# Kernel tuning notes

Hardware: AMD Instinct MI355X
Metric: run time of the kernel (lower is better)

## Reference

```python
import jax, jax.numpy as jnp
import numpy as np

B, C_IN, IMG, P, G, E, H = 4, 3, 576, 16, 36, 768, 12
T = G * G  # 1296 tokens
HD = E // H  # 64
LN_EPS = 1e-5


def layer_norm(x, g, b):
    mu = jnp.mean(x, axis=-1, keepdims=True)
    var = jnp.mean((x - mu) ** 2, axis=-1, keepdims=True)
    return (x - mu) * jax.lax.rsqrt(var + LN_EPS) * g + b


def setup_inputs() -> dict:
    key = jax.random.key(0)
    ks = jax.random.split(key, 12)
    s = lambda *sh: 0.02
    return {
        "x": jax.random.normal(ks[0], (B, C_IN, IMG, IMG), jnp.float32),
        "conv_w": jax.random.normal(ks[1], (E, C_IN, P, P), jnp.float32) * 0.02,
        "conv_b": jnp.zeros((E,), jnp.float32),
        "wq": jax.random.normal(ks[2], (E, E), jnp.float32) * 0.02,
        "wk": jax.random.normal(ks[3], (E, E), jnp.float32) * 0.02,
        "wv": jax.random.normal(ks[4], (E, E), jnp.float32) * 0.02,
        "wo": jax.random.normal(ks[5], (E, E), jnp.float32) * 0.02,
        "bo": jnp.zeros((E,), jnp.float32),
        "w1": jax.random.normal(ks[6], (E, 4 * E), jnp.float32) * 0.02,
        "b1": jnp.zeros((4 * E,), jnp.float32),
        "w2": jax.random.normal(ks[7], (4 * E, E), jnp.float32) * 0.02,
        "b2": jnp.zeros((E,), jnp.float32),
        "ln1_g": jnp.ones((E,), jnp.float32),
        "ln1_b": jnp.zeros((E,), jnp.float32),
        "ln2_g": jnp.ones((E,), jnp.float32),
        "ln2_b": jnp.zeros((E,), jnp.float32),
    }


def reference(x, conv_w, conv_b, wq, wk, wv, wo, bo, w1, b1, w2, b2,
              ln1_g, ln1_b, ln2_g, ln2_b):
    # --- patch embed: stride==kernel conv as patch reshape + einsum ---
    xr = x.reshape(B, C_IN, G, P, G, P)  # b c i p j q
    tok = jnp.einsum('bcipjq,ecpq->bije', xr, conv_w) + conv_b
    tok = tok.reshape(B, T, E)  # row-major (i,j) matches flatten(2).transpose

    # --- causal multi-head attention (scale uses n_embd, as in source) ---
    h = layer_norm(tok, ln1_g, ln1_b)
    q = (h @ wq).reshape(B, T, H, HD)
    k = (h @ wk).reshape(B, T, H, HD)
    v = (h @ wv).reshape(B, T, H, HD)
    scores = jnp.einsum('bqhd,bkhd->bhqk', q, k) * (E ** -0.5)
    mask = jnp.tril(jnp.ones((T, T), bool))
    scores = jnp.where(mask, scores, -jnp.inf)
    attn = jax.nn.softmax(scores, axis=-1)
    ao = jnp.einsum('bhqk,bkhd->bqhd', attn, v).reshape(B, T, E)
    tok = tok + (ao @ wo + bo)

    # --- MLP ---
    h2 = layer_norm(tok, ln2_g, ln2_b)
    tok = tok + (jax.nn.relu(h2 @ w1 + b1) @ w2 + b2)

    # --- back to image grid ---
    return tok.reshape(B, G, G, E).transpose(0, 3, 1, 2)
```

## Files before the change

### kernel.cpp

```cpp
#include <hip/hip_runtime.h>

typedef unsigned short u16;
typedef unsigned int u32;
typedef unsigned long long u64;
typedef float f32x4 __attribute__((ext_vector_type(4)));
typedef __bf16 bf16x8 __attribute__((ext_vector_type(8)));
typedef u16 u16x8 __attribute__((ext_vector_type(8)));

#define DEV __device__ __forceinline__


DEV u16 f2bf(float f) {
    union { float f; u32 u; } un; un.f = f;
    u32 u = un.u;
    return (u16)((u + 0x7fffu + ((u >> 16) & 1u)) >> 16);
}

DEV void gll16(const u16* src, u16* dst) {
    auto g = (const __attribute__((address_space(1))) u32*)(src);
    auto s = (__attribute__((address_space(3))) u32*)(dst);
    __builtin_amdgcn_global_load_lds(g, s, 16, 0, 0);
}

__global__ void convcvt_k(const float* __restrict__ src, u16* __restrict__ dst) {
    int i = blockIdx.x * 256 + threadIdx.x;
    f32x4 v = ((const f32x4*)src)[i];
    union { u16 q[4]; u64 ll; } un;
    #pragma unroll
    for (int j = 0; j < 4; ++j) un.q[j] = f2bf(v[j]);
    ((u64*)dst)[i] = un.ll;
}

__global__ void wtrans_k(const float* __restrict__ src, u16* __restrict__ dst, int K, int N) {
    __shared__ float tile[32][33];
    int n0 = blockIdx.x * 32, k0 = blockIdx.y * 32;
    int tx = threadIdx.x & 31, ty = threadIdx.x >> 5;
    #pragma unroll
    for (int i = 0; i < 32; i += 8)
        tile[ty + i][tx] = src[(size_t)(k0 + ty + i) * N + n0 + tx];
    __syncthreads();
    #pragma unroll
    for (int i = 0; i < 32; i += 8)
        dst[(size_t)(n0 + ty + i) * K + k0 + tx] = f2bf(tile[tx][ty + i]);
}

__global__ void patch_k(const float* __restrict__ x, u16* __restrict__ out) {
    int idx = blockIdx.x * 256 + threadIdx.x;
    int j = idx % 36; int r1 = idx / 36;
    int p = r1 % 16;  int r2 = r1 / 16;
    int i = r2 % 36;  int r3 = r2 / 36;
    int c = r3 % 3;   int b = r3 / 3;
    const f32x4* src = (const f32x4*)(x + (size_t)((b * 3 + c) * 576 + i * 16 + p) * 576 + j * 16);
    u16x8 lo, hi;
    #pragma unroll
    for (int k = 0; k < 2; ++k) {
        f32x4 v = src[k];
        #pragma unroll
        for (int e = 0; e < 4; ++e) lo[k * 4 + e] = f2bf(v[e]);
    }
    #pragma unroll
    for (int k = 0; k < 2; ++k) {
        f32x4 v = src[2 + k];
        #pragma unroll
        for (int e = 0; e < 4; ++e) hi[k * 4 + e] = f2bf(v[e]);
    }
    u16* dst = out + (size_t)(b * 1296 + i * 36 + j) * 768 + c * 256 + p * 16;
    *(u16x8*)dst = lo;
    *(u16x8*)(dst + 8) = hi;
}

__global__ __launch_bounds__(256) void ln_k(const float* __restrict__ x, const float* __restrict__ g,
                                            const float* __restrict__ bta, u16* __restrict__ out) {
    int row = blockIdx.x * 4 + (threadIdx.x >> 6);
    int l = threadIdx.x & 63;
    const float* xr = x + (size_t)row * 768;
    float v[12]; float s = 0.f, s2 = 0.f;
    #pragma unroll
    for (int i = 0; i < 12; ++i) { v[i] = xr[l + 64 * i]; s += v[i]; s2 += v[i] * v[i]; }
    #pragma unroll
    for (int off = 32; off; off >>= 1) { s += __shfl_xor(s, off); s2 += __shfl_xor(s2, off); }
    float mu = s * (1.f / 768.f);
    float var = s2 * (1.f / 768.f) - mu * mu;
    float rs = rsqrtf(var + 1e-5f);
    u16* orow = out + (size_t)row * 768;
    #pragma unroll
    for (int i = 0; i < 12; ++i) {
        int c = l + 64 * i;
        orow[c] = f2bf((v[i] - mu) * rs * g[c] + bta[c]);
    }
}

__global__ void vtrans_k(const u16* __restrict__ qkv, u16* __restrict__ vt) {
    __shared__ u16 tile[32][33];
    int bh = blockIdx.z; int b = bh / 12, h = bh % 12;
    int t0 = blockIdx.x * 32, d0 = blockIdx.y * 32;
    int tx = threadIdx.x & 31, ty = threadIdx.x >> 5;
    #pragma unroll
    for (int i = 0; i < 32; i += 8) {
        int t = t0 + ty + i; int tc = min(t, 1295);
        tile[ty + i][tx] = qkv[(size_t)(b * 1296 + tc) * 2304 + 1536 + h * 64 + d0 + tx];
    }
    __syncthreads();
    #pragma unroll
    for (int i = 0; i < 32; i += 8) {
        int d = d0 + ty + i; int t = t0 + tx;
        if (t < 1296) vt[(size_t)(bh * 64 + d) * 1344 + t] = tile[tx][ty + i];
    }
}

template <int BN, int EPI>
__global__ __launch_bounds__(256) void gemm_k(const u16* __restrict__ A, const u16* __restrict__ Bt,
                                              const float* __restrict__ bias, const float* __restrict__ resid,
                                              void* __restrict__ Cout, int K, int ldc) {
    constexpr int M = 5184;
    constexpr int NF = BN / 32;
    __shared__ __align__(16) u16 lds[2][4096 + BN * 32];
    const int tid = threadIdx.x;
    const int l = tid & 63, w = tid >> 6;
    const int lr = l & 15, lq = l >> 4;
    const int wm = w >> 1, wn = w & 1;
    const int bm = blockIdx.y * 128;
    const int bn = blockIdx.x * BN;
    const int ar = l >> 2;
    const int ap = l & 3;

    f32x4 acc[4][NF];
    f32x4 zz = {0.f, 0.f, 0.f, 0.f};
    #pragma unroll
    for (int i = 0; i < 4; ++i)
        #pragma unroll
        for (int j = 0; j < NF; ++j) acc[i][j] = zz;

    const int nk = K >> 5;

    auto stage = [&](int buf, int kt) {
        #pragma unroll
        for (int i = 0; i < 2; ++i) {
            int c = 2 * w + i;
            int row = c * 16 + ar;
            int piece = ap ^ (row & 3);
            const u16* src = A + (size_t)min(bm + row, M - 1) * K + kt * 32 + piece * 8;
            gll16(src, &lds[buf][c * 512]);
        }
        if constexpr (BN == 128) {
            #pragma unroll
            for (int i = 0; i < 2; ++i) {
                int c = 2 * w + i;
                int row = c * 16 + ar;
                int piece = ap ^ (row & 3);
                const u16* src = Bt + (size_t)(bn + row) * K + kt * 32 + piece * 8;
                gll16(src, &lds[buf][4096 + c * 512]);
            }
        } else {
            int c = w;
            int row = c * 16 + ar;
            int piece = ap ^ (row & 3);
            const u16* src = Bt + (size_t)(bn + row) * K + kt * 32 + piece * 8;
            gll16(src, &lds[buf][4096 + c * 512]);
        }
    };

    stage(0, 0);
    __syncthreads();
    for (int kt = 0; kt < nk; ++kt) {
        int cur = kt & 1;
        if (kt + 1 < nk) stage(cur ^ 1, kt + 1);
        bf16x8 af[4], bfr[NF];
        #pragma unroll
        for (int mi = 0; mi < 4; ++mi) {
            int row = wm * 64 + mi * 16 + lr;
            af[mi] = *(const bf16x8*)&lds[cur][row * 32 + (lq ^ (row & 3)) * 8];
        }
        #pragma unroll
        for (int ni = 0; ni < NF; ++ni) {
            int row = wn * (BN / 2) + ni * 16 + lr;
            bfr[ni] = *(const bf16x8*)&lds[cur][4096 + row * 32 + (lq ^ (row & 3)) * 8];
        }
        #pragma unroll
        for (int mi = 0; mi < 4; ++mi)
            #pragma unroll
            for (int ni = 0; ni < NF; ++ni)
                acc[mi][ni] = __builtin_amdgcn_mfma_f32_16x16x32_bf16(af[mi], bfr[ni], acc[mi][ni], 0, 0, 0);
        __syncthreads();
    }

    #pragma unroll
    for (int mi = 0; mi < 4; ++mi) {
        #pragma unroll
        for (int ni = 0; ni < NF; ++ni) {
            int col = bn + wn * (BN / 2) + ni * 16 + lr;
            float bv = 0.f;
            if constexpr (EPI != 1) bv = bias[col];
            #pragma unroll
            for (int r = 0; r < 4; ++r) {
                int m = bm + wm * 64 + mi * 16 + 4 * lq + r;
                if (m < M) {
                    float v = acc[mi][ni][r] + bv;
                    if constexpr (EPI == 2) v = fmaxf(v, 0.f);
                    if constexpr (EPI == 3 || EPI == 4) v += resid[(size_t)m * ldc + col];
                    if constexpr (EPI == 0 || EPI == 3) {
                        ((float*)Cout)[(size_t)m * ldc + col] = v;
                    } else if constexpr (EPI == 4) {
                        int b = m / 1296, t = m - b * 1296;
                        ((float*)Cout)[(size_t)(b * 768 + col) * 1296 + t] = v;
                    } else {
                        ((u16*)Cout)[(size_t)m * ldc + col] = f2bf(v);
                    }
                }
            }
        }
    }
}

__global__ __launch_bounds__(256, 2) void attn_k(const u16* __restrict__ qkv, const u16* __restrict__ vt,
                                                 u16* __restrict__ ao) {
    const float SCALE = 0.03608439182435161f;
    __shared__ __align__(16) u16 kv[2][2][4096];
    __shared__ __align__(16) u16 plds[4][16 * 72];
    const int tid = threadIdx.x;
    const int wid = tid >> 6, l = tid & 63;
    const int id = blockIdx.x;
    const int xr = id & 7, sl = id >> 3;
    const int g = sl / 11, bx = sl - g * 11;
    const int bh = g * 8 + xr;
    const int b = bh / 12, h = bh % 12;
    const int uu = bx * 4 + wid;
    const int u = min(uu, 40);
    const bool valid = (uu <= 40);
    const int lr = l & 15, lq = l >> 4;
    const int q0S = 16 * u, q0L = 16 * (80 - u);
    const bool hasS = valid && (u < 40);
    const int nktS = (u < 40) ? (((q0S + 15) >> 6) + 1) : 0;
    const int nktL = ((q0L + 15) >> 6) + 1;
    const int umin = min(bx * 4, 40);
    const int nktmax = ((16 * (80 - umin) + 15) >> 6) + 1;

    const u16* kbase = qkv + (size_t)(b * 1296) * 2304 + 768 + h * 64;
    const u16* vbase = vt + (size_t)bh * 64 * 1344;
    u16* pl = &plds[wid][0];

    const u16* qpS = qkv + (size_t)(b * 1296 + q0S + lr) * 2304 + h * 64;
    const u16* qpL = qkv + (size_t)(b * 1296 + q0L + lr) * 2304 + h * 64;
    bf16x8 qS0 = *(const bf16x8*)(qpS + 8 * lq);
    bf16x8 qS1 = *(const bf16x8*)(qpS + 32 + 8 * lq);
    bf16x8 qL0 = *(const bf16x8*)(qpL + 8 * lq);
    bf16x8 qL1 = *(const bf16x8*)(qpL + 32 + 8 * lq);

    f32x4 zz = {0.f, 0.f, 0.f, 0.f};
    f32x4 oS[4], oL[4];
    float mS[4], mL[4], lSs[4], lLs[4];
    #pragma unroll
    for (int i = 0; i < 4; ++i) {
        oS[i] = zz; oL[i] = zz;
        mS[i] = -__builtin_inff(); mL[i] = -__builtin_inff();
        lSs[i] = 0.f; lLs[i] = 0.f;
    }

    auto stage = [&](int buf, int kt) {
        const int k0 = kt * 64;
        #pragma unroll
        for (int i = 0; i < 2; ++i) {
            int slot = tid + i * 256;
            int row = slot >> 3;
            int piece = slot & 7;
            int sp = piece ^ (row & 7);
            int tc = min(k0 + row, 1295);
            gll16(kbase + (size_t)tc * 2304 + sp * 8,
                  &kv[buf][0][((tid & 0xFFFFFFC0) + i * 256) * 8]);
        }
        #pragma unroll
        for (int i = 0; i < 2; ++i) {
            int slot = tid + i * 256;
            int row = slot >> 3;
            int piece = slot & 7;
            int sp = piece ^ (row & 7);
            gll16(vbase + (size_t)row * 1344 + k0 + sp * 8,
                  &kv[buf][1][((tid & 0xFFFFFFC0) + i * 256) * 8]);
        }
    };

    bf16x8 kb[4][2], vb[4][2];

    auto visit = [&](int q0, bf16x8 qa0, bf16x8 qa1, f32x4 (&o)[4],
                     float (&mrow)[4], float (&lsum)[4], int k0) {
        f32x4 s[4];
        #pragma unroll
        for (int nt = 0; nt < 4; ++nt) {
            f32x4 a = zz;
            a = __builtin_amdgcn_mfma_f32_16x16x32_bf16(qa0, kb[nt][0], a, 0, 0, 0);
            a = __builtin_amdgcn_mfma_f32_16x16x32_bf16(qa1, kb[nt][1], a, 0, 0, 0);
            s[nt] = a;
        }
        float tmax[4];
        #pragma unroll
        for (int r = 0; r < 4; ++r) {
            int qrow = q0 + 4 * lq + r;
            #pragma unroll
            for (int nt = 0; nt < 4; ++nt) {
                int tcol = k0 + nt * 16 + lr;
                float val = s[nt][r] * SCALE;
                s[nt][r] = (tcol <= qrow) ? val : -__builtin_inff();
            }
            tmax[r] = fmaxf(fmaxf(s[0][r], s[1][r]), fmaxf(s[2][r], s[3][r]));
        }
        #pragma unroll
        for (int off = 1; off < 16; off <<= 1)
            #pragma unroll
            for (int r = 0; r < 4; ++r) tmax[r] = fmaxf(tmax[r], __shfl_xor(tmax[r], off));
        float alpha[4], tsum[4];
        #pragma unroll
        for (int r = 0; r < 4; ++r) {
            float nm = fmaxf(mrow[r], tmax[r]);
            alpha[r] = __expf(mrow[r] - nm);
            mrow[r] = nm;
            float accp = 0.f;
            #pragma unroll
            for (int nt = 0; nt < 4; ++nt) {
                float p = __expf(s[nt][r] - nm);
                s[nt][r] = p;
                accp += p;
            }
            tsum[r] = accp;
        }
        #pragma unroll
        for (int off = 1; off < 16; off <<= 1)
            #pragma unroll
            for (int r = 0; r < 4; ++r) tsum[r] += __shfl_xor(tsum[r], off);
        #pragma unroll
        for (int r = 0; r < 4; ++r) lsum[r] = lsum[r] * alpha[r] + tsum[r];
        #pragma unroll
        for (int dt = 0; dt < 4; ++dt)
            #pragma unroll
            for (int r = 0; r < 4; ++r) o[dt][r] *= alpha[r];
        #pragma unroll
        for (int nt = 0; nt < 4; ++nt)
            #pragma unroll
            for (int r = 0; r < 4; ++r)
                pl[(4 * lq + r) * 72 + nt * 16 + lr] = f2bf(s[nt][r]);
        __builtin_amdgcn_wave_barrier();
        bf16x8 pa0 = *(const bf16x8*)&pl[lr * 72 + 8 * lq];
        bf16x8 pa1 = *(const bf16x8*)&pl[lr * 72 + 32 + 8 * lq];
        #pragma unroll
        for (int dt = 0; dt < 4; ++dt) {
            o[dt] = __builtin_amdgcn_mfma_f32_16x16x32_bf16(pa0, vb[dt][0], o[dt], 0, 0, 0);
            o[dt] = __builtin_amdgcn_mfma_f32_16x16x32_bf16(pa1, vb[dt][1], o[dt], 0, 0, 0);
        }
        __builtin_amdgcn_wave_barrier();
    };

    stage(0, 0);
    for (int kt = 0; kt < nktmax; ++kt) {
        const int cur = kt & 1;
        const int k0 = kt * 64;
        __syncthreads();
        if (kt + 1 < nktmax) stage(cur ^ 1, kt + 1);
        #pragma unroll
        for (int nt = 0; nt < 4; ++nt) {
            int krow = nt * 16 + lr;
            kb[nt][0] = *(const bf16x8*)&kv[cur][0][krow * 64 + ((lq ^ (krow & 7)) << 3)];
            kb[nt][1] = *(const bf16x8*)&kv[cur][0][krow * 64 + (((lq + 4) ^ (krow & 7)) << 3)];
        }
        #pragma unroll
        for (int dt = 0; dt < 4; ++dt) {
            int vrow = dt * 16 + lr;
            vb[dt][0] = *(const bf16x8*)&kv[cur][1][vrow * 64 + ((lq ^ (vrow & 7)) << 3)];
            vb[dt][1] = *(const bf16x8*)&kv[cur][1][vrow * 64 + (((lq + 4) ^ (vrow & 7)) << 3)];
        }
        if (valid && kt < nktS) visit(q0S, qS0, qS1, oS, mS, lSs, k0);
        if (valid && kt < nktL) visit(q0L, qL0, qL1, oL, mL, lLs, k0);
    }

    if (valid) {
        #pragma unroll
        for (int dt = 0; dt < 4; ++dt)
            #pragma unroll
            for (int r = 0; r < 4; ++r) {
                if (hasS) {
                    int qrow = q0S + 4 * lq + r;
                    ao[(size_t)(b * 1296 + qrow) * 768 + h * 64 + dt * 16 + lr] = f2bf(oS[dt][r] / lSs[r]);
                }
                int qrowL = q0L + 4 * lq + r;
                ao[(size_t)(b * 1296 + qrowL) * 768 + h * 64 + dt * 16 + lr] = f2bf(oL[dt][r] / lLs[r]);
            }
    }
}

extern "C" void kernel_launch(void* const* d_in, const int* in_sizes, int n_in,
                              void* d_out, int out_size, void* d_ws, size_t ws_size,
                              hipStream_t stream) {
    const float* x      = (const float*)d_in[0];
    const float* conv_w = (const float*)d_in[1];
    const float* conv_b = (const float*)d_in[2];
    const float* wq     = (const float*)d_in[3];
    const float* wk     = (const float*)d_in[4];
    const float* wv     = (const float*)d_in[5];
    const float* wo     = (const float*)d_in[6];
    const float* bo     = (const float*)d_in[7];
    const float* w1     = (const float*)d_in[8];
    const float* b1     = (const float*)d_in[9];
    const float* w2     = (const float*)d_in[10];
    const float* b2     = (const float*)d_in[11];
    const float* ln1g   = (const float*)d_in[12];
    const float* ln1b   = (const float*)d_in[13];
    const float* ln2g   = (const float*)d_in[14];
    const float* ln2b   = (const float*)d_in[15];

    char* ws = (char*)d_ws;
    size_t off = 0;
    auto alloc = [&](size_t bytes) { char* p = ws + off; off = (off + bytes + 255) & ~(size_t)255; return p; };
    u16*   convw_bf = (u16*)alloc((size_t)768 * 768 * 2);
    u16*   wqkv_t   = (u16*)alloc((size_t)2304 * 768 * 2);
    u16*   wo_t     = (u16*)alloc((size_t)768 * 768 * 2);
    u16*   w1_t     = (u16*)alloc((size_t)3072 * 768 * 2);
    u16*   w2_t     = (u16*)alloc((size_t)768 * 3072 * 2);
    float* tok      = (float*)alloc((size_t)5184 * 768 * 4);
    u16*   hbuf     = (u16*)alloc((size_t)5184 * 768 * 2);
    u16*   apao     = (u16*)alloc((size_t)5184 * 768 * 2);
    size_t qkv_bytes = ((size_t)5184 * 2304 * 2 + 255) & ~(size_t)255;
    size_t vt_bytes  = (size_t)48 * 64 * 1344 * 2;
    size_t a1_bytes  = (size_t)5184 * 3072 * 2;
    size_t big_bytes = qkv_bytes + vt_bytes;
    if (a1_bytes > big_bytes) big_bytes = a1_bytes;
    char* big = alloc(big_bytes);
    u16* qkvb = (u16*)big;
    u16* vtb  = (u16*)(big + qkv_bytes);
    u16* a1   = (u16*)big;

    convcvt_k<<<576, 256, 0, stream>>>(conv_w, convw_bf);
    wtrans_k<<<dim3(24, 24), 256, 0, stream>>>(wq, wqkv_t, 768, 768);
    wtrans_k<<<dim3(24, 24), 256, 0, stream>>>(wk, wqkv_t + 768 * 768, 768, 768);
    wtrans_k<<<dim3(24, 24), 256, 0, stream>>>(wv, wqkv_t + 2 * 768 * 768, 768, 768);
    wtrans_k<<<dim3(24, 24), 256, 0, stream>>>(wo, wo_t, 768, 768);
    wtrans_k<<<dim3(96, 24), 256, 0, stream>>>(w1, w1_t, 768, 3072);
    wtrans_k<<<dim3(24, 96), 256, 0, stream>>>(w2, w2_t, 3072, 768);
    patch_k<<<972, 256, 0, stream>>>(x, apao);
    gemm_k<64, 0><<<dim3(12, 41), 256, 0, stream>>>(apao, convw_bf, conv_b, nullptr, tok, 768, 768);
    ln_k<<<1296, 256, 0, stream>>>(tok, ln1g, ln1b, hbuf);
    gemm_k<128, 1><<<dim3(18, 41), 256, 0, stream>>>(hbuf, wqkv_t, nullptr, nullptr, qkvb, 768, 2304);
    vtrans_k<<<dim3(41, 2, 48), 256, 0, stream>>>(qkvb, vtb);
    attn_k<<<528, 256, 0, stream>>>(qkvb, vtb, apao);
    gemm_k<64, 3><<<dim3(12, 41), 256, 0, stream>>>(apao, wo_t, bo, tok, tok, 768, 768);
    ln_k<<<1296, 256, 0, stream>>>(tok, ln2g, ln2b, hbuf);
    gemm_k<128, 2><<<dim3(24, 41), 256, 0, stream>>>(hbuf, w1_t, b1, nullptr, a1, 768, 3072);
    gemm_k<64, 4><<<dim3(12, 41), 256, 0, stream>>>(a1, w2_t, b2, tok, d_out, 3072, 768);
}
```

Baseline: 383.6 us.

## Double GEMM K-tile to 64 with 8-way swizzle and XCD-aware block remap

The GEMM kernel now stages a 64-wide K slice per iteration instead of 32, using an 8-piece XOR swizzle in LDS and issuing two MFMAs per fragment pair. This halves the number of barrier and stage iterations. The grid is also flattened to 1D and remapped so that consecutive work tiles land on the same XCD (blockIdx mod 8), which should improve L2 reuse of shared A and B panels. In exchange, LDS use doubles, which may lower occupancy, and register pressure rises from the doubled fragment arrays.

```diff
diff --git a/kernel.cpp b/kernel.cpp
--- a/kernel.cpp
+++ b/kernel.cpp
@@ -111,52 +111,51 @@
 template <int BN, int EPI>
 __global__ __launch_bounds__(256) void gemm_k(const u16* __restrict__ A, const u16* __restrict__ Bt,
                                               const float* __restrict__ bias, const float* __restrict__ resid,
-                                              void* __restrict__ Cout, int K, int ldc) {
+                                              void* __restrict__ Cout, int K, int ldc, int nbx) {
     constexpr int M = 5184;
     constexpr int NF = BN / 32;
-    __shared__ __align__(16) u16 lds[2][4096 + BN * 32];
+    __shared__ __align__(16) u16 lds[2][(128 + BN) * 64];
     const int tid = threadIdx.x;
     const int l = tid & 63, w = tid >> 6;
     const int lr = l & 15, lq = l >> 4;
     const int wm = w >> 1, wn = w & 1;
-    const int bm = blockIdx.y * 128;
-    const int bn = blockIdx.x * BN;
-    const int ar = l >> 2;
-    const int ap = l & 3;
+
+    const int total = nbx * 41;
+    const int q = total >> 3, r = total & 7;
+    const int x = blockIdx.x & 7;
+    const int j = blockIdx.x >> 3;
+    const int wrk = x * q + min(x, r) + j;
+    const int by = wrk / nbx, bx = wrk - by * nbx;
+    const int bm = by * 128;
+    const int bn = bx * BN;
 
     f32x4 acc[4][NF];
     f32x4 zz = {0.f, 0.f, 0.f, 0.f};
     #pragma unroll
     for (int i = 0; i < 4; ++i)
         #pragma unroll
-        for (int j = 0; j < NF; ++j) acc[i][j] = zz;
-
-    const int nk = K >> 5;
+        for (int jj = 0; jj < NF; ++jj) acc[i][jj] = zz;
+
+    const int nk = K >> 6;
 
     auto stage = [&](int buf, int kt) {
-        #pragma unroll
-        for (int i = 0; i < 2; ++i) {
-            int c = 2 * w + i;
-            int row = c * 16 + ar;
-            int piece = ap ^ (row & 3);
-            const u16* src = A + (size_t)min(bm + row, M - 1) * K + kt * 32 + piece * 8;
-            gll16(src, &lds[buf][c * 512]);
-        }
-        if constexpr (BN == 128) {
-            #pragma unroll
-            for (int i = 0; i < 2; ++i) {
-                int c = 2 * w + i;
-                int row = c * 16 + ar;
-                int piece = ap ^ (row & 3);
-                const u16* src = Bt + (size_t)(bn + row) * K + kt * 32 + piece * 8;
-                gll16(src, &lds[buf][4096 + c * 512]);
-            }
-        } else {
-            int c = w;
-            int row = c * 16 + ar;
-            int piece = ap ^ (row & 3);
-            const u16* src = Bt + (size_t)(bn + row) * K + kt * 32 + piece * 8;
-            gll16(src, &lds[buf][4096 + c * 512]);
+        u16* abase = &lds[buf][0];
+        #pragma unroll
+        for (int i = 0; i < 4; ++i) {
+            int slot = tid + i * 256;
+            int row = slot >> 3, piece = slot & 7;
+            int sp = piece ^ (row & 7);
+            const u16* src = A + (size_t)min(bm + row, M - 1) * K + kt * 64 + sp * 8;
+            gll16(src, abase + ((tid & ~63) + i * 256) * 8);
+        }
+        u16* bbase = &lds[buf][128 * 64];
+        #pragma unroll
+        for (int i = 0; i < NF; ++i) {
+            int slot = tid + i * 256;
+            int row = slot >> 3, piece = slot & 7;
+            int sp = piece ^ (row & 7);
+            const u16* src = Bt + (size_t)(bn + row) * K + kt * 64 + sp * 8;
+            gll16(src, bbase + ((tid & ~63) + i * 256) * 8);
         }
     };
 
@@ -165,22 +164,28 @@
     for (int kt = 0; kt < nk; ++kt) {
         int cur = kt & 1;
         if (kt + 1 < nk) stage(cur ^ 1, kt + 1);
-        bf16x8 af[4], bfr[NF];
+        bf16x8 af[4][2], bfr[NF][2];
         #pragma unroll
         for (int mi = 0; mi < 4; ++mi) {
             int row = wm * 64 + mi * 16 + lr;
-            af[mi] = *(const bf16x8*)&lds[cur][row * 32 + (lq ^ (row & 3)) * 8];
+            #pragma unroll
+            for (int ks = 0; ks < 2; ++ks)
+                af[mi][ks] = *(const bf16x8*)&lds[cur][row * 64 + (((lq + 4 * ks) ^ (row & 7)) << 3)];
         }
         #pragma unroll
         for (int ni = 0; ni < NF; ++ni) {
             int row = wn * (BN / 2) + ni * 16 + lr;
-            bfr[ni] = *(const bf16x8*)&lds[cur][4096 + row * 32 + (lq ^ (row & 3)) * 8];
+            #pragma unroll
+            for (int ks = 0; ks < 2; ++ks)
+                bfr[ni][ks] = *(const bf16x8*)&lds[cur][128 * 64 + row * 64 + (((lq + 4 * ks) ^ (row & 7)) << 3)];
         }
         #pragma unroll
         for (int mi = 0; mi < 4; ++mi)
             #pragma unroll
-            for (int ni = 0; ni < NF; ++ni)
-                acc[mi][ni] = __builtin_amdgcn_mfma_f32_16x16x32_bf16(af[mi], bfr[ni], acc[mi][ni], 0, 0, 0);
+            for (int ni = 0; ni < NF; ++ni) {
+                acc[mi][ni] = __builtin_amdgcn_mfma_f32_16x16x32_bf16(af[mi][0], bfr[ni][0], acc[mi][ni], 0, 0, 0);
+                acc[mi][ni] = __builtin_amdgcn_mfma_f32_16x16x32_bf16(af[mi][1], bfr[ni][1], acc[mi][ni], 0, 0, 0);
+            }
         __syncthreads();
     }
 
@@ -192,10 +197,10 @@
             float bv = 0.f;
             if constexpr (EPI != 1) bv = bias[col];
             #pragma unroll
-            for (int r = 0; r < 4; ++r) {
-                int m = bm + wm * 64 + mi * 16 + 4 * lq + r;
+            for (int rr = 0; rr < 4; ++rr) {
+                int m = bm + wm * 64 + mi * 16 + 4 * lq + rr;
                 if (m < M) {
-                    float v = acc[mi][ni][r] + bv;
+                    float v = acc[mi][ni][rr] + bv;
                     if constexpr (EPI == 2) v = fmaxf(v, 0.f);
                     if constexpr (EPI == 3 || EPI == 4) v += resid[(size_t)m * ldc + col];
                     if constexpr (EPI == 0 || EPI == 3) {
@@ -434,13 +439,13 @@
     wtrans_k<<<dim3(96, 24), 256, 0, stream>>>(w1, w1_t, 768, 3072);
     wtrans_k<<<dim3(24, 96), 256, 0, stream>>>(w2, w2_t, 3072, 768);
     patch_k<<<972, 256, 0, stream>>>(x, apao);
-    gemm_k<64, 0><<<dim3(12, 41), 256, 0, stream>>>(apao, convw_bf, conv_b, nullptr, tok, 768, 768);
+    gemm_k<64, 0><<<12 * 41, 256, 0, stream>>>(apao, convw_bf, conv_b, nullptr, tok, 768, 768, 12);
     ln_k<<<1296, 256, 0, stream>>>(tok, ln1g, ln1b, hbuf);
-    gemm_k<128, 1><<<dim3(18, 41), 256, 0, stream>>>(hbuf, wqkv_t, nullptr, nullptr, qkvb, 768, 2304);
+    gemm_k<128, 1><<<18 * 41, 256, 0, stream>>>(hbuf, wqkv_t, nullptr, nullptr, qkvb, 768, 2304, 18);
     vtrans_k<<<dim3(41, 2, 48), 256, 0, stream>>>(qkvb, vtb);
     attn_k<<<528, 256, 0, stream>>>(qkvb, vtb, apao);
-    gemm_k<64, 3><<<dim3(12, 41), 256, 0, stream>>>(apao, wo_t, bo, tok, tok, 768, 768);
+    gemm_k<64, 3><<<12 * 41, 256, 0, stream>>>(apao, wo_t, bo, tok, tok, 768, 768, 12);
     ln_k<<<1296, 256, 0, stream>>>(tok, ln2g, ln2b, hbuf);
-    gemm_k<128, 2><<<dim3(24, 41), 256, 0, stream>>>(hbuf, w1_t, b1, nullptr, a1, 768, 3072);
-    gemm_k<64, 4><<<dim3(12, 41), 256, 0, stream>>>(a1, w2_t, b2, tok, d_out, 3072, 768);
-}
+    gemm_k<128, 2><<<24 * 41, 256, 0, stream>>>(hbuf, w1_t, b1, nullptr, a1, 768, 3072, 24);
+    gemm_k<64, 4><<<12 * 41, 256, 0, stream>>>(a1, w2_t, b2, tok, d_out, 3072, 768, 12);
+}
```

Result: faster. 350.8 us (-8.5%).
